# Kernel tuning notes

Hardware: AMD Instinct MI355X
Metric: run time of the kernel (lower is better)

## Reference

```python
import jax, jax.numpy as jnp
import numpy as np


def setup_inputs() -> dict:
    key = jax.random.key(0)
    k1, k2 = jax.random.split(key)
    B, L, D = 8, 2048, 128
    query = jax.random.normal(k1, (B, L, D), dtype=jnp.float32)
    value = jax.random.normal(k2, (B, L, D), dtype=jnp.float32)
    return {"query": query, "value": value}


def reference(query, value):
    # scores: [B, Lq, Lk] = query @ value^T (note: NO 1/sqrt(d) scaling, key == value)
    scores = jnp.einsum("bqd,bkd->bqk", query, value)
    weights = jax.nn.softmax(scores, axis=-1)
    # context: [B, Lq, D]
    context = jnp.einsum("bqk,bkd->bqd", weights, value)
    return context
```

## Files before the change

kernel.cpp:

```cpp
#include <hip/hip_runtime.h>
#include <hip/hip_fp16.h>

typedef _Float16 f16;
typedef __attribute__((ext_vector_type(8))) _Float16 f16x8;
typedef __attribute__((ext_vector_type(4))) _Float16 f16x4;
typedef __attribute__((ext_vector_type(4))) short s16x4;
typedef __attribute__((ext_vector_type(4))) float f32x4;
typedef __attribute__((ext_vector_type(2))) float f32x2;

#define MFMA16(a,b,c) __builtin_amdgcn_mfma_f32_16x16x32_f16(a,b,c,0,0,0)
#define EXP2(x) __builtin_amdgcn_exp2f(x)
#define LOG2E 1.4426950408889634f

#define B_DIM 8
#define L_DIM 2048
#define D_DIM 128
#define NGRP 4
#define KVB 64
#define NTILES 8
#define TILE_B 16384
#define P_ST 72
#define SLAB_ST 132
#define SMEM_B 137216

__device__ __forceinline__ unsigned ldsa(const void* p) {
    return (unsigned)(unsigned long long)(const __attribute__((address_space(3))) char*)p;
}

#define TRRD(d, a, O) asm volatile("ds_read_b64_tr_b16 %0, %1 offset:" O : "=v"(d) : "v"(a))
#define LGKM0() do { asm volatile("s_waitcnt lgkmcnt(0)" ::: "memory"); __builtin_amdgcn_sched_barrier(0); } while (0)
#define GLDS(gp, lp) __builtin_amdgcn_global_load_lds( \
    (const __attribute__((address_space(1))) unsigned int*)(gp), \
    (__attribute__((address_space(3))) unsigned int*)(lp), 16, 0, 0)

#define PVND(TL, TH, PA0, PA1, ND) { \
    union { s16x4 s2[2]; f16x8 v; } uu; uu.s2[0] = TL; uu.s2[1] = TH; \
    acc[0][ND] = MFMA16(PA0, uu.v, acc[0][ND]); \
    acc[1][ND] = MFMA16(PA1, uu.v, acc[1][ND]); }

#define PV_HALF(AREG, PA0, PA1, S0,S0b,S1,S1b,S2,S2b,S3,S3b, NDB) { \
    s16x4 t0l,t0h,t1l,t1h,t2l,t2h,t3l,t3h; \
    TRRD(t0l, AREG, S0);  TRRD(t0h, AREG, S0b); \
    TRRD(t1l, AREG, S1);  TRRD(t1h, AREG, S1b); \
    TRRD(t2l, AREG, S2);  TRRD(t2h, AREG, S2b); \
    TRRD(t3l, AREG, S3);  TRRD(t3h, AREG, S3b); \
    LGKM0(); \
    __builtin_amdgcn_s_setprio(1); \
    PVND(t0l, t0h, PA0, PA1, NDB+0); PVND(t1l, t1h, PA0, PA1, NDB+1); \
    PVND(t2l, t2h, PA0, PA1, NDB+2); PVND(t3l, t3h, PA0, PA1, NDB+3); \
    __builtin_amdgcn_s_setprio(0); }

__global__ __launch_bounds__(256) void prep_v(const float* __restrict__ V, f16* __restrict__ ws) {
    const int blk = blockIdx.x;
    const float* src = V + (size_t)blk * (KVB * D_DIM);
    f16* dst = ws + (size_t)blk * (KVB * D_DIM);
    const int t = threadIdx.x;
    #pragma unroll
    for (int ii = 0; ii < 4; ++ii) {
        int lin = ii * 256 + t;
        int kv = lin >> 4, oct = lin & 15;
        const float* sp = src + kv * D_DIM + oct * 8;
        f32x4 a = *(const f32x4*)sp;
        f32x4 b = *(const f32x4*)(sp + 4);
        int c = (kv >> 2) * 64 + (oct >> 1) * 8 + (kv & 3) * 2 + (oct & 1);
        union { f16 h[8]; f16x8 v; } u;
        #pragma unroll
        for (int k = 0; k < 4; ++k) { u.h[k] = (f16)a[k]; u.h[k + 4] = (f16)b[k]; }
        *(f16x8*)(dst + (size_t)c * 8) = u.v;
    }
}

__global__ __launch_bounds__(512, 2) void attn_fwd(
    const float* __restrict__ Q, const f16* __restrict__ ws, float* __restrict__ Out)
{
    __shared__ __align__(16) char smem[SMEM_B];

    const int tid  = threadIdx.x;
    const int wv   = tid >> 6;
    const int grp  = wv >> 1;
    const int qw   = wv & 1;
    const int lane = tid & 63;
    const int lrow = lane & 15;
    const int g    = lane >> 4;

    const int blk = blockIdx.x;
    const int b   = blk & 7;
    const int q0  = (blk >> 3) * 64;

    char* grpbase = smem + grp * (2 * TILE_B);

    f16x8 qhi[2][4], qlo[2][4];
    {
        const float* qb = Q + ((size_t)b * L_DIM + q0 + qw * 32) * D_DIM;
        #pragma unroll
        for (int q2 = 0; q2 < 2; ++q2) {
            const float* qp = qb + (size_t)(q2 * 16 + lrow) * D_DIM + g * 8;
            #pragma unroll
            for (int dt = 0; dt < 4; ++dt) {
                f32x4 f0 = *(const f32x4*)(qp + dt * 32);
                f32x4 f1 = *(const f32x4*)(qp + dt * 32 + 4);
                #pragma unroll
                for (int i = 0; i < 4; ++i) {
                    float s0 = f0[i] * LOG2E;
                    f16 h0 = (f16)s0;
                    qhi[q2][dt][i] = h0;
                    qlo[q2][dt][i] = (f16)(s0 - (float)h0);
                    float s1 = f1[i] * LOG2E;
                    f16 h1 = (f16)s1;
                    qhi[q2][dt][i + 4] = h1;
                    qlo[q2][dt][i + 4] = (f16)(s1 - (float)h1);
                }
            }
        }
    }

    f32x4 acc[2][8];
    #pragma unroll
    for (int q2 = 0; q2 < 2; ++q2)
        #pragma unroll
        for (int i = 0; i < 8; ++i) acc[q2][i] = (f32x4)0.0f;
    float m_run[2] = { -3.0e38f, -3.0e38f }, l_run[2] = { 0.0f, 0.0f };

    const int qkoff = (lrow >> 2) * 1024 + (g >> 1) * 128 + (lrow & 3) * 32 + (g & 1) * 16;

    const f16* wsb = ws + (size_t)b * (32 * KVB * D_DIM);

    {
        const f16* w0 = wsb + (size_t)(grp * 8) * 8192 + (size_t)(qw * 512 + lane) * 8;
        char* ldst = grpbase + qw * 8192;
        #pragma unroll
        for (int i = 0; i < 8; ++i) GLDS(w0 + i * 512, ldst + i * 1024);
    }
    __syncthreads();

    for (int t = 0; t < NTILES; ++t) {
        const int c = t & 1;
        char* cur = grpbase + c * TILE_B;
        char* alt = grpbase + (c ^ 1) * TILE_B;

        f32x4 s[2][4];
        #pragma unroll
        for (int q2 = 0; q2 < 2; ++q2)
            #pragma unroll
            for (int nt = 0; nt < 4; ++nt) s[q2][nt] = (f32x4)0.0f;
        __builtin_amdgcn_s_setprio(1);
        #pragma unroll
        for (int nt = 0; nt < 4; ++nt) {
            #pragma unroll
            for (int dt = 0; dt < 4; ++dt) {
                f16x8 a = *(const f16x8*)(cur + qkoff + nt * 4096 + dt * 256);
                s[0][nt] = MFMA16(a, qhi[0][dt], s[0][nt]);
                s[0][nt] = MFMA16(a, qlo[0][dt], s[0][nt]);
                s[1][nt] = MFMA16(a, qhi[1][dt], s[1][nt]);
                s[1][nt] = MFMA16(a, qlo[1][dt], s[1][nt]);
            }
        }
        __builtin_amdgcn_s_setprio(0);

        float pm[2];
        #pragma unroll
        for (int q2 = 0; q2 < 2; ++q2) {
            float tm = s[q2][0][0];
            #pragma unroll
            for (int nt = 0; nt < 4; ++nt)
                #pragma unroll
                for (int r = 0; r < 4; ++r) tm = fmaxf(tm, s[q2][nt][r]);
            tm = fmaxf(tm, __shfl_xor(tm, 16));
            tm = fmaxf(tm, __shfl_xor(tm, 32));
            pm[q2] = tm;
        }
        bool need = (pm[0] > m_run[0] + 11.5f) || (pm[1] > m_run[1] + 11.5f);
        if (__any(need)) {
            float scl[2];
            #pragma unroll
            for (int q2 = 0; q2 < 2; ++q2) {
                float mnew = fmaxf(m_run[q2], pm[q2]);
                scl[q2]  = EXP2(m_run[q2] - mnew);
                m_run[q2] = mnew;
                l_run[q2] *= scl[q2];
            }
            float sr[2][4];
            #pragma unroll
            for (int r = 0; r < 4; ++r) {
                sr[0][r] = __shfl(scl[0], g * 4 + r);
                sr[1][r] = __shfl(scl[1], g * 4 + r);
            }
            #pragma unroll
            for (int q2 = 0; q2 < 2; ++q2)
                #pragma unroll
                for (int nd = 0; nd < 8; ++nd)
                    #pragma unroll
                    for (int r = 0; r < 4; ++r) acc[q2][nd][r] *= sr[q2][r];
        }
        #pragma unroll
        for (int q2 = 0; q2 < 2; ++q2) {
            float ps = 0.0f;
            #pragma unroll
            for (int nt = 0; nt < 4; ++nt)
                #pragma unroll
                for (int r = 0; r < 4; ++r) {
                    float p = EXP2(s[q2][nt][r] - m_run[q2]);
                    s[q2][nt][r] = p;
                    ps += p;
                }
            ps += __shfl_xor(ps, 16);
            ps += __shfl_xor(ps, 32);
            l_run[q2] += ps;
        }

        f16* pls = (f16*)(alt + qw * 8192);
        #pragma unroll
        for (int q2 = 0; q2 < 2; ++q2) {
            #pragma unroll
            for (int nt = 0; nt < 4; ++nt) {
                f16x4 w = { (f16)s[q2][nt][0], (f16)s[q2][nt][1],
                            (f16)s[q2][nt][2], (f16)s[q2][nt][3] };
                *(f16x4*)(pls + (size_t)(q2 * 16 + lrow) * P_ST + nt * 16 + g * 4) = w;
            }
        }
        f16x8 pa00, pa01, pa10, pa11;
        pa00 = *(const f16x8*)(pls + (size_t)(lrow) * P_ST + g * 8);
        pa01 = *(const f16x8*)(pls + (size_t)(lrow) * P_ST + 32 + g * 8);
        pa10 = *(const f16x8*)(pls + (size_t)(16 + lrow) * P_ST + g * 8);
        pa11 = *(const f16x8*)(pls + (size_t)(16 + lrow) * P_ST + 32 + g * 8);
        LGKM0();

        if (t + 1 < NTILES) {
            const f16* wnt = wsb + (size_t)(grp * 8 + t + 1) * 8192 + (size_t)(qw * 512 + lane) * 8;
            char* ldst = alt + qw * 8192;
            #pragma unroll
            for (int i = 0; i < 8; ++i) GLDS(wnt + i * 512, ldst + i * 1024);
        }

        unsigned atr0 = ldsa(cur) + (unsigned)(g * 2048 + lrow * 8);
        unsigned atr1 = atr0 + 8192u;
        PV_HALF(atr0, pa00, pa10, "0","1024","128","1152","256","1280","384","1408", 0);
        PV_HALF(atr0, pa00, pa10, "512","1536","640","1664","768","1792","896","1920", 4);
        PV_HALF(atr1, pa01, pa11, "0","1024","128","1152","256","1280","384","1408", 0);
        PV_HALF(atr1, pa01, pa11, "512","1536","640","1664","768","1792","896","1920", 4);

        __syncthreads();
    }

    float* slab = (float*)smem;
    float* mlp  = (float*)(smem + 8 * 32 * SLAB_ST * 4);
    #pragma unroll
    for (int q2 = 0; q2 < 2; ++q2)
        #pragma unroll
        for (int nd = 0; nd < 8; ++nd)
            #pragma unroll
            for (int r = 0; r < 4; ++r)
                slab[(size_t)(wv * 32 + q2 * 16 + g * 4 + r) * SLAB_ST + nd * 16 + lrow] = acc[q2][nd][r];
    if (g == 0) {
        #pragma unroll
        for (int q2 = 0; q2 < 2; ++q2) {
            mlp[wv * 64 + q2 * 16 + lrow]      = m_run[q2];
            mlp[wv * 64 + 32 + q2 * 16 + lrow] = l_run[q2];
        }
    }
    __syncthreads();

    #pragma unroll
    for (int rr = 0; rr < 8; ++rr) {
        int row = wv * 8 + rr;
        int qws = row >> 5, ql = row & 31;
        float mg[4], M = -3.0e38f;
        #pragma unroll
        for (int gg = 0; gg < 4; ++gg) {
            mg[gg] = mlp[(gg * 2 + qws) * 64 + ql];
            M = fmaxf(M, mg[gg]);
        }
        float L = 0.0f, f[4];
        #pragma unroll
        for (int gg = 0; gg < 4; ++gg) {
            f[gg] = EXP2(mg[gg] - M);
            L += f[gg] * mlp[(gg * 2 + qws) * 64 + 32 + ql];
        }
        float inv = 1.0f / L;
        f32x2 o = { 0.0f, 0.0f };
        #pragma unroll
        for (int gg = 0; gg < 4; ++gg) {
            f32x2 v = *(const f32x2*)&slab[(size_t)((gg * 2 + qws) * 32 + ql) * SLAB_ST + lane * 2];
            o[0] += f[gg] * v[0];
            o[1] += f[gg] * v[1];
        }
        o[0] *= inv; o[1] *= inv;
        *(f32x2*)&Out[((size_t)b * L_DIM + q0 + row) * D_DIM + lane * 2] = o;
    }
}

extern "C" void kernel_launch(void* const* d_in, const int* in_sizes, int n_in,
                              void* d_out, int out_size, void* d_ws, size_t ws_size,
                              hipStream_t stream) {
    const float* Q = (const float*)d_in[0];
    const float* V = (const float*)d_in[1];
    float* Out     = (float*)d_out;
    f16* ws        = (f16*)d_ws;
    prep_v<<<dim3(B_DIM * (L_DIM / KVB)), dim3(256), 0, stream>>>(V, ws);
    attn_fwd<<<dim3(B_DIM * (L_DIM / 64)), dim3(512), 0, stream>>>(Q, ws, Out);
}
```

Before: 41.39 us.

## Store pre-transposed V copy and halve KV tile to drop transpose reads

The prep kernel now writes two fp16 copies of each V tile: the QK-layout copy and a pre-transposed D-major copy, staged through LDS. The attention kernel halves the KV block to 32 rows and doubles the tile count. It reads the transposed copy with plain 16-byte LDS loads instead of ds_read_b64_tr_b16 transpose reads, cutting per-tile reads and waits in the PV step. In exchange the workspace traffic doubles, each tile does less work, and there are twice as many loop iterations and barriers.

```diff
diff --git a/kernel.cpp b/kernel.cpp
--- a/kernel.cpp
+++ b/kernel.cpp
@@ -4,7 +4,6 @@
 typedef _Float16 f16;
 typedef __attribute__((ext_vector_type(8))) _Float16 f16x8;
 typedef __attribute__((ext_vector_type(4))) _Float16 f16x4;
-typedef __attribute__((ext_vector_type(4))) short s16x4;
 typedef __attribute__((ext_vector_type(4))) float f32x4;
 typedef __attribute__((ext_vector_type(2))) float f32x2;
 
@@ -16,10 +15,11 @@
 #define L_DIM 2048
 #define D_DIM 128
 #define NGRP 4
-#define KVB 64
-#define NTILES 8
+#define KVB 32
+#define NTILES 16
 #define TILE_B 16384
-#define P_ST 72
+#define TILE_H 8192
+#define P_ST 40
 #define SLAB_ST 132
 #define SMEM_B 137216
 
@@ -27,46 +27,42 @@
     return (unsigned)(unsigned long long)(const __attribute__((address_space(3))) char*)p;
 }
 
-#define TRRD(d, a, O) asm volatile("ds_read_b64_tr_b16 %0, %1 offset:" O : "=v"(d) : "v"(a))
 #define LGKM0() do { asm volatile("s_waitcnt lgkmcnt(0)" ::: "memory"); __builtin_amdgcn_sched_barrier(0); } while (0)
 #define GLDS(gp, lp) __builtin_amdgcn_global_load_lds( \
     (const __attribute__((address_space(1))) unsigned int*)(gp), \
     (__attribute__((address_space(3))) unsigned int*)(lp), 16, 0, 0)
 
-#define PVND(TL, TH, PA0, PA1, ND) { \
-    union { s16x4 s2[2]; f16x8 v; } uu; uu.s2[0] = TL; uu.s2[1] = TH; \
-    acc[0][ND] = MFMA16(PA0, uu.v, acc[0][ND]); \
-    acc[1][ND] = MFMA16(PA1, uu.v, acc[1][ND]); }
-
-#define PV_HALF(AREG, PA0, PA1, S0,S0b,S1,S1b,S2,S2b,S3,S3b, NDB) { \
-    s16x4 t0l,t0h,t1l,t1h,t2l,t2h,t3l,t3h; \
-    TRRD(t0l, AREG, S0);  TRRD(t0h, AREG, S0b); \
-    TRRD(t1l, AREG, S1);  TRRD(t1h, AREG, S1b); \
-    TRRD(t2l, AREG, S2);  TRRD(t2h, AREG, S2b); \
-    TRRD(t3l, AREG, S3);  TRRD(t3h, AREG, S3b); \
-    LGKM0(); \
-    __builtin_amdgcn_s_setprio(1); \
-    PVND(t0l, t0h, PA0, PA1, NDB+0); PVND(t1l, t1h, PA0, PA1, NDB+1); \
-    PVND(t2l, t2h, PA0, PA1, NDB+2); PVND(t3l, t3h, PA0, PA1, NDB+3); \
-    __builtin_amdgcn_s_setprio(0); }
-
 __global__ __launch_bounds__(256) void prep_v(const float* __restrict__ V, f16* __restrict__ ws) {
+    __shared__ f16 lds[KVB * D_DIM];
     const int blk = blockIdx.x;
     const float* src = V + (size_t)blk * (KVB * D_DIM);
-    f16* dst = ws + (size_t)blk * (KVB * D_DIM);
+    f16* dst = ws + (size_t)blk * TILE_H;
     const int t = threadIdx.x;
     #pragma unroll
-    for (int ii = 0; ii < 4; ++ii) {
-        int lin = ii * 256 + t;
-        int kv = lin >> 4, oct = lin & 15;
-        const float* sp = src + kv * D_DIM + oct * 8;
-        f32x4 a = *(const f32x4*)sp;
-        f32x4 b = *(const f32x4*)(sp + 4);
-        int c = (kv >> 2) * 64 + (oct >> 1) * 8 + (kv & 3) * 2 + (oct & 1);
+    for (int i = 0; i < 4; ++i) {
+        int idx4 = (i * 256 + t) * 4;
+        f32x4 f = *(const f32x4*)(src + idx4);
+        f16x4 h = { (f16)f[0], (f16)f[1], (f16)f[2], (f16)f[3] };
+        *(f16x4*)(lds + idx4) = h;
+    }
+    __syncthreads();
+    #pragma unroll
+    for (int i = 0; i < 2; ++i) {
+        int c = i * 256 + t;
+        int kvblk = c >> 6, w = c & 63;
+        int d16 = w >> 3, r2 = w & 7;
+        int kv = kvblk * 4 + (r2 >> 1), d0 = d16 * 16 + (r2 & 1) * 8;
+        f16x8 v = *(const f16x8*)(lds + kv * D_DIM + d0);
+        *(f16x8*)(dst + c * 8) = v;
+    }
+    #pragma unroll
+    for (int i = 0; i < 2; ++i) {
+        int cc = i * 256 + t;
+        int d = cc >> 2, k8 = (cc & 3) * 8;
         union { f16 h[8]; f16x8 v; } u;
         #pragma unroll
-        for (int k = 0; k < 4; ++k) { u.h[k] = (f16)a[k]; u.h[k + 4] = (f16)b[k]; }
-        *(f16x8*)(dst + (size_t)c * 8) = u.v;
+        for (int j = 0; j < 8; ++j) u.h[j] = lds[(k8 + j) * D_DIM + d];
+        *(f16x8*)(dst + 4096 + cc * 8) = u.v;
     }
 }
 
@@ -123,13 +119,13 @@
 
     const int qkoff = (lrow >> 2) * 1024 + (g >> 1) * 128 + (lrow & 3) * 32 + (g & 1) * 16;
 
-    const f16* wsb = ws + (size_t)b * (32 * KVB * D_DIM);
+    const f16* wsb = ws + (size_t)b * (64 * TILE_H);
 
     {
-        const f16* w0 = wsb + (size_t)(grp * 8) * 8192 + (size_t)(qw * 512 + lane) * 8;
-        char* ldst = grpbase + qw * 8192;
-        #pragma unroll
-        for (int i = 0; i < 8; ++i) GLDS(w0 + i * 512, ldst + i * 1024);
+        const f16* w0 = wsb + (size_t)(grp * NTILES) * TILE_H + qw * 4096 + lane * 8;
+        char* l0 = grpbase + qw * 8192;
+        #pragma unroll
+        for (int i = 0; i < 8; ++i) GLDS(w0 + i * 512, l0 + i * 1024);
     }
     __syncthreads();
 
@@ -138,14 +134,14 @@
         char* cur = grpbase + c * TILE_B;
         char* alt = grpbase + (c ^ 1) * TILE_B;
 
-        f32x4 s[2][4];
+        f32x4 s[2][2];
         #pragma unroll
         for (int q2 = 0; q2 < 2; ++q2)
             #pragma unroll
-            for (int nt = 0; nt < 4; ++nt) s[q2][nt] = (f32x4)0.0f;
+            for (int nt = 0; nt < 2; ++nt) s[q2][nt] = (f32x4)0.0f;
         __builtin_amdgcn_s_setprio(1);
         #pragma unroll
-        for (int nt = 0; nt < 4; ++nt) {
+        for (int nt = 0; nt < 2; ++nt) {
             #pragma unroll
             for (int dt = 0; dt < 4; ++dt) {
                 f16x8 a = *(const f16x8*)(cur + qkoff + nt * 4096 + dt * 256);
@@ -162,7 +158,7 @@
         for (int q2 = 0; q2 < 2; ++q2) {
             float tm = s[q2][0][0];
             #pragma unroll
-            for (int nt = 0; nt < 4; ++nt)
+            for (int nt = 0; nt < 2; ++nt)
                 #pragma unroll
                 for (int r = 0; r < 4; ++r) tm = fmaxf(tm, s[q2][nt][r]);
             tm = fmaxf(tm, __shfl_xor(tm, 16));
@@ -196,7 +192,7 @@
         for (int q2 = 0; q2 < 2; ++q2) {
             float ps = 0.0f;
             #pragma unroll
-            for (int nt = 0; nt < 4; ++nt)
+            for (int nt = 0; nt < 2; ++nt)
                 #pragma unroll
                 for (int r = 0; r < 4; ++r) {
                     float p = EXP2(s[q2][nt][r] - m_run[q2]);
@@ -212,32 +208,32 @@
         #pragma unroll
         for (int q2 = 0; q2 < 2; ++q2) {
             #pragma unroll
-            for (int nt = 0; nt < 4; ++nt) {
+            for (int nt = 0; nt < 2; ++nt) {
                 f16x4 w = { (f16)s[q2][nt][0], (f16)s[q2][nt][1],
                             (f16)s[q2][nt][2], (f16)s[q2][nt][3] };
                 *(f16x4*)(pls + (size_t)(q2 * 16 + lrow) * P_ST + nt * 16 + g * 4) = w;
             }
         }
-        f16x8 pa00, pa01, pa10, pa11;
-        pa00 = *(const f16x8*)(pls + (size_t)(lrow) * P_ST + g * 8);
-        pa01 = *(const f16x8*)(pls + (size_t)(lrow) * P_ST + 32 + g * 8);
-        pa10 = *(const f16x8*)(pls + (size_t)(16 + lrow) * P_ST + g * 8);
-        pa11 = *(const f16x8*)(pls + (size_t)(16 + lrow) * P_ST + 32 + g * 8);
+        f16x8 pa0 = *(const f16x8*)(pls + (size_t)(lrow) * P_ST + g * 8);
+        f16x8 pa1 = *(const f16x8*)(pls + (size_t)(16 + lrow) * P_ST + g * 8);
         LGKM0();
 
         if (t + 1 < NTILES) {
-            const f16* wnt = wsb + (size_t)(grp * 8 + t + 1) * 8192 + (size_t)(qw * 512 + lane) * 8;
+            const f16* wnt = wsb + (size_t)(grp * NTILES + t + 1) * TILE_H + qw * 4096 + lane * 8;
             char* ldst = alt + qw * 8192;
             #pragma unroll
             for (int i = 0; i < 8; ++i) GLDS(wnt + i * 512, ldst + i * 1024);
         }
 
-        unsigned atr0 = ldsa(cur) + (unsigned)(g * 2048 + lrow * 8);
-        unsigned atr1 = atr0 + 8192u;
-        PV_HALF(atr0, pa00, pa10, "0","1024","128","1152","256","1280","384","1408", 0);
-        PV_HALF(atr0, pa00, pa10, "512","1536","640","1664","768","1792","896","1920", 4);
-        PV_HALF(atr1, pa01, pa11, "0","1024","128","1152","256","1280","384","1408", 0);
-        PV_HALF(atr1, pa01, pa11, "512","1536","640","1664","768","1792","896","1920", 4);
+        const char* vt = cur + 8192;
+        __builtin_amdgcn_s_setprio(1);
+        #pragma unroll
+        for (int nd = 0; nd < 8; ++nd) {
+            f16x8 bf = *(const f16x8*)(vt + (nd * 16 + lrow) * 64 + g * 16);
+            acc[0][nd] = MFMA16(pa0, bf, acc[0][nd]);
+            acc[1][nd] = MFMA16(pa1, bf, acc[1][nd]);
+        }
+        __builtin_amdgcn_s_setprio(0);
 
         __syncthreads();
     }
```

Result: slower. 49.78 us (+20.3%).

## Replace block-wide barriers with per-group LDS flag handshakes for K/V tile pipeline

Applied to the files above, without the earlier changes.

Each loop iteration used to end in a block-wide __syncthreads. That is replaced by per-group, per-buffer LDS flags: the two waves of a group poll a 'tile loaded' flag before computing and a 'buffer consumed' flag before reissuing global_load_lds into the alternate buffer. The P staging area moves to a dedicated per-wave LDS region, written in two 16-row halves, so it no longer aliases the alternate K/V buffer. The aim is to decouple the four groups and remove the cost of full-block barriers. In exchange, LDS use grows, which may hurt the two-blocks-per-CU occupancy. Spin-polling on volatile LDS flags also carries memory-ordering risk, since the LDS writes from global_load_lds may not be visible to the other wave when the flag is set.

```diff
diff --git a/kernel.cpp b/kernel.cpp
--- a/kernel.cpp
+++ b/kernel.cpp
@@ -15,13 +15,15 @@
 #define B_DIM 8
 #define L_DIM 2048
 #define D_DIM 128
-#define NGRP 4
 #define KVB 64
 #define NTILES 8
 #define TILE_B 16384
 #define P_ST 72
+#define PLS_OFF 131072
+#define PLS_W 2304
+#define FLG_OFF 149504
 #define SLAB_ST 132
-#define SMEM_B 137216
+#define SMEM_B 149760
 
 __device__ __forceinline__ unsigned ldsa(const void* p) {
     return (unsigned)(unsigned long long)(const __attribute__((address_space(3))) char*)p;
@@ -32,6 +34,17 @@
 #define GLDS(gp, lp) __builtin_amdgcn_global_load_lds( \
     (const __attribute__((address_space(1))) unsigned int*)(gp), \
     (__attribute__((address_space(3))) unsigned int*)(lp), 16, 0, 0)
+
+__device__ __forceinline__ void poll_ge(int* p, int need) {
+    volatile int* vp = (volatile int*)p;
+    while (*vp < need) __builtin_amdgcn_s_sleep(1);
+    asm volatile("" ::: "memory");
+    __builtin_amdgcn_sched_barrier(0);
+}
+__device__ __forceinline__ void flag_set(int* p, int v) {
+    asm volatile("" ::: "memory");
+    *(volatile int*)p = v;
+}
 
 #define PVND(TL, TH, PA0, PA1, ND) { \
     union { s16x4 s2[2]; f16x8 v; } uu; uu.s2[0] = TL; uu.s2[1] = TH; \
@@ -88,6 +101,7 @@
     const int q0  = (blk >> 3) * 64;
 
     char* grpbase = smem + grp * (2 * TILE_B);
+    int*  fl      = (int*)(smem + FLG_OFF) + grp * 8;
 
     f16x8 qhi[2][4], qlo[2][4];
     {
@@ -122,21 +136,29 @@
     float m_run[2] = { -3.0e38f, -3.0e38f }, l_run[2] = { 0.0f, 0.0f };
 
     const int qkoff = (lrow >> 2) * 1024 + (g >> 1) * 128 + (lrow & 3) * 32 + (g & 1) * 16;
-
     const f16* wsb = ws + (size_t)b * (32 * KVB * D_DIM);
+
+    if (tid < 32) ((int*)(smem + FLG_OFF))[tid] = 0;
+    __syncthreads();
 
     {
         const f16* w0 = wsb + (size_t)(grp * 8) * 8192 + (size_t)(qw * 512 + lane) * 8;
         char* ldst = grpbase + qw * 8192;
         #pragma unroll
         for (int i = 0; i < 8; ++i) GLDS(w0 + i * 512, ldst + i * 1024);
-    }
-    __syncthreads();
+        asm volatile("s_waitcnt vmcnt(0)" ::: "memory");
+        if (lane == 0) flag_set(fl + 0 * 4 + qw * 2 + 0, 1);
+    }
+
+    f16* pls = (f16*)(smem + PLS_OFF + wv * PLS_W);
 
     for (int t = 0; t < NTILES; ++t) {
-        const int c = t & 1;
-        char* cur = grpbase + c * TILE_B;
-        char* alt = grpbase + (c ^ 1) * TILE_B;
+        const int cb = t & 1, ab = cb ^ 1;
+        char* cur = grpbase + cb * TILE_B;
+        char* alt = grpbase + ab * TILE_B;
+
+        poll_ge(fl + cb * 4 + 0, t + 1);
+        poll_ge(fl + cb * 4 + 2, t + 1);
 
         f32x4 s[2][4];
         #pragma unroll
@@ -208,24 +230,31 @@
             l_run[q2] += ps;
         }
 
-        f16* pls = (f16*)(alt + qw * 8192);
-        #pragma unroll
-        for (int q2 = 0; q2 < 2; ++q2) {
+        f16x8 pa00, pa01, pa10, pa11;
+        {
             #pragma unroll
             for (int nt = 0; nt < 4; ++nt) {
-                f16x4 w = { (f16)s[q2][nt][0], (f16)s[q2][nt][1],
-                            (f16)s[q2][nt][2], (f16)s[q2][nt][3] };
-                *(f16x4*)(pls + (size_t)(q2 * 16 + lrow) * P_ST + nt * 16 + g * 4) = w;
-            }
-        }
-        f16x8 pa00, pa01, pa10, pa11;
-        pa00 = *(const f16x8*)(pls + (size_t)(lrow) * P_ST + g * 8);
-        pa01 = *(const f16x8*)(pls + (size_t)(lrow) * P_ST + 32 + g * 8);
-        pa10 = *(const f16x8*)(pls + (size_t)(16 + lrow) * P_ST + g * 8);
-        pa11 = *(const f16x8*)(pls + (size_t)(16 + lrow) * P_ST + 32 + g * 8);
-        LGKM0();
+                f16x4 w = { (f16)s[0][nt][0], (f16)s[0][nt][1],
+                            (f16)s[0][nt][2], (f16)s[0][nt][3] };
+                *(f16x4*)(pls + (size_t)lrow * P_ST + nt * 16 + g * 4) = w;
+            }
+            pa00 = *(const f16x8*)(pls + (size_t)lrow * P_ST + g * 8);
+            pa01 = *(const f16x8*)(pls + (size_t)lrow * P_ST + 32 + g * 8);
+            LGKM0();
+            #pragma unroll
+            for (int nt = 0; nt < 4; ++nt) {
+                f16x4 w = { (f16)s[1][nt][0], (f16)s[1][nt][1],
+                            (f16)s[1][nt][2], (f16)s[1][nt][3] };
+                *(f16x4*)(pls + (size_t)lrow * P_ST + nt * 16 + g * 4) = w;
+            }
+            pa10 = *(const f16x8*)(pls + (size_t)lrow * P_ST + g * 8);
+            pa11 = *(const f16x8*)(pls + (size_t)lrow * P_ST + 32 + g * 8);
+            LGKM0();
+        }
 
         if (t + 1 < NTILES) {
+            poll_ge(fl + ab * 4 + 1, t);
+            poll_ge(fl + ab * 4 + 3, t);
             const f16* wnt = wsb + (size_t)(grp * 8 + t + 1) * 8192 + (size_t)(qw * 512 + lane) * 8;
             char* ldst = alt + qw * 8192;
             #pragma unroll
@@ -239,8 +268,14 @@
         PV_HALF(atr1, pa01, pa11, "0","1024","128","1152","256","1280","384","1408", 0);
         PV_HALF(atr1, pa01, pa11, "512","1536","640","1664","768","1792","896","1920", 4);
 
-        __syncthreads();
-    }
+        if (lane == 0) flag_set(fl + cb * 4 + qw * 2 + 1, t + 1);
+        if (t + 1 < NTILES) {
+            asm volatile("s_waitcnt vmcnt(0)" ::: "memory");
+            if (lane == 0) flag_set(fl + ab * 4 + qw * 2 + 0, t + 2);
+        }
+    }
+
+    __syncthreads();
 
     float* slab = (float*)smem;
     float* mlp  = (float*)(smem + 8 * 32 * SLAB_ST * 4);
```

Measured after the change: 43.79 us. +5.8%, slower.
